# Performance work log

Hardware: AMD Instinct MI355X
Metric: run time of the kernel (lower is better)

Reference implementation:

```python
import jax, jax.numpy as jnp
import numpy as np

B, T, D_IN, D, K, H, BAND = 4, 1536, 512, 512, 2, 8, 24
DH = D // H
ALPHA, BETA, EPS = 6.0, 0.5, 1e-5


def _ln(x, g, b):
    m = x.mean(-1, keepdims=True)
    v = ((x - m) ** 2).mean(-1, keepdims=True)
    return (x - m) / jnp.sqrt(v + EPS) * g + b


def setup_inputs() -> dict:
    key = jax.random.key(0)
    ks = jax.random.split(key, 16)
    sc = 0.02
    inp = {
        "x_m": jax.random.normal(ks[0], (B, T, D_IN), jnp.float32),
        "A": jax.random.uniform(ks[1], (B, T, K), jnp.float32),
        "W_in": jax.random.normal(ks[2], (D_IN, D), jnp.float32) * sc,
        "b_in": jnp.zeros((D,), jnp.float32),
        "ln_q_g": jnp.ones((D,), jnp.float32), "ln_q_b": jnp.zeros((D,), jnp.float32),
        "ln_kv_g": jnp.ones((D,), jnp.float32), "ln_kv_b": jnp.zeros((D,), jnp.float32),
        "Wq": jax.random.normal(ks[3], (D, D), jnp.float32) * sc,
        "bq": jnp.zeros((D,), jnp.float32),
        "Wk": jax.random.normal(ks[4], (D, D), jnp.float32) * sc,
        "bk": jnp.zeros((D,), jnp.float32),
        "Wv": jax.random.normal(ks[5], (D, D), jnp.float32) * sc,
        "bv": jnp.zeros((D,), jnp.float32),
        "Wo": jax.random.normal(ks[6], (D, D), jnp.float32) * sc,
        "bo": jnp.zeros((D,), jnp.float32),
        "ln_f_g": jnp.ones((D,), jnp.float32), "ln_f_b": jnp.zeros((D,), jnp.float32),
        "W1": jax.random.normal(ks[7], (D, 4 * D), jnp.float32) * sc,
        "b1": jnp.zeros((4 * D,), jnp.float32),
        "W2": jax.random.normal(ks[8], (4 * D, D), jnp.float32) * sc,
        "b2": jnp.zeros((D,), jnp.float32),
        "ln_s_g": jnp.ones((D,), jnp.float32), "ln_s_b": jnp.zeros((D,), jnp.float32),
        "spk_tags": jax.random.normal(ks[9], (K, D), jnp.float32) / np.sqrt(D),
    }
    return inp


def reference(x_m, A, W_in, b_in, ln_q_g, ln_q_b, ln_kv_g, ln_kv_b,
              Wq, bq, Wk, bk, Wv, bv, Wo, bo,
              ln_f_g, ln_f_b, W1, b1, W2, b2, ln_s_g, ln_s_b, spk_tags):
    X = x_m @ W_in + b_in                      # [B,T,D]
    W_hat = jax.nn.sigmoid(ALPHA * (A - BETA))  # [B,T,K] sigmoid gating

    # banded additive mask (|i-j| <= BAND allowed)
    idx = jnp.arange(T)
    allowed = jnp.abs(idx[:, None] - idx[None, :]) <= BAND
    mask = jnp.where(allowed, 0.0, -jnp.inf).astype(X.dtype)  # [T,T]

    # K/V come from the (shared) mixed memory X
    KV = _ln(X, ln_kv_g, ln_kv_b)
    k_p = (KV @ Wk + bk).reshape(B, T, H, DH)
    v_p = (KV @ Wv + bv).reshape(B, T, H, DH)

    streams = []
    for kk in range(K):
        Xk = X * W_hat[..., kk:kk + 1]
        Q = _ln(Xk, ln_q_g, ln_q_b)
        q = (Q @ Wq + bq).reshape(B, T, H, DH)
        scores = jnp.einsum('bthd,bshd->bhts', q, k_p) / np.sqrt(DH) + mask
        p = jax.nn.softmax(scores, axis=-1)
        y = jnp.einsum('bhts,bshd->bthd', p, v_p).reshape(B, T, D) @ Wo + bo
        y = Xk + y                              # residual after attention
        h = _ln(y, ln_f_g, ln_f_b)
        h = jax.nn.gelu(h @ W1 + b1, approximate=False) @ W2 + b2
        out_k = y + h + spk_tags[kk]            # ffn residual + speaker tag
        out_k = _ln(out_k, ln_s_g, ln_s_b)      # per-stream LayerNorm
        streams.append(out_k)
    return jnp.concatenate(streams, axis=1)    # [B, K*T, D]
```

## Files before the change

kernel.cpp:

```cpp
#include <hip/hip_runtime.h>
#include <hip/hip_bf16.h>
#include <math.h>

#define B_    4
#define T_    1536
#define DIN_  512
#define D_    512
#define K_    2
#define H_    8
#define BAND_ 24
#define DH_   64
#define M_    (B_*T_)
#define M2_   (2*M_)
#define ALPHA_ 6.0f
#define BETA_  0.5f
#define EPS_   1e-5f

using bf8  = __attribute__((ext_vector_type(8))) short;
using f32x4 = __attribute__((ext_vector_type(4))) float;

__device__ __forceinline__ void async_copy16(const void* g, void* l) {
  __builtin_amdgcn_global_load_lds(
      (const __attribute__((address_space(1))) unsigned int*)g,
      (__attribute__((address_space(3))) unsigned int*)l, 16, 0, 0);
}

__device__ __forceinline__ short f2bf(float v) {
  __hip_bfloat16 h = (__hip_bfloat16)v;
  return *(short*)&h;
}
__device__ __forceinline__ float bf2f(short s) {
  union { unsigned u; float f; } c;
  c.u = ((unsigned)(unsigned short)s) << 16;
  return c.f;
}
__device__ __forceinline__ int swz64(int row, int col) {
  return (col & ~63) | ((((col >> 3) ^ row) & 7) << 3) | (col & 7);
}
__device__ __forceinline__ float fast_gelu(float x) {
  const float t = fmaf(0.1029504013f, x * x, 2.3021170686f);
  const float e = __builtin_amdgcn_exp2f(x * t);
  const float r = __builtin_amdgcn_rcpf(e + 1.0f);
  return fmaf(-x, r, x);
}

template<int BM, int BN, int NI, int NJ, int FLAGS>
__global__ __launch_bounds__(256) void gemm_bt_t(
    const short* __restrict__ A, const short* __restrict__ Bt,
    const float* __restrict__ bias, const void* __restrict__ res,
    const float* __restrict__ tag2,
    void* __restrict__ Cout, int M, int N, int Kd, int gx) {
  __shared__ short lA[BM * 64];
  __shared__ short lB[BN * 64];
  const int gy   = gridDim.x / gx;
  const int xcd  = blockIdx.x & 7;
  const int seq  = blockIdx.x >> 3;
  const int rpx  = gy >> 3;
  const int by   = xcd * rpx + seq / gx;
  const int bx   = seq % gx;
  const int tid  = threadIdx.x;
  const int wave = tid >> 6, lane = tid & 63;
  const int block_m = by * BM, block_n = bx * BN;
  const int wm = (wave & 1) * (BM / 2), wn = (wave >> 1) * (BN / 2);
  const int l15 = lane & 15, quad = lane >> 4, l7 = lane & 7;
  f32x4 acc[NI][NJ] = {};

  for (int k0 = 0; k0 < Kd; k0 += 64) {
    __syncthreads();
#pragma unroll
    for (int i = 0; i < BM / 32; ++i) {
      const int cb = wave * (BM * 2) + i * 64;
      const int c  = cb + lane;
      async_copy16(A + (size_t)(block_m + (c >> 3)) * Kd + k0 + (c & 7) * 8,
                   &lA[cb * 8]);
    }
#pragma unroll
    for (int i = 0; i < BN / 32; ++i) {
      const int cb = wave * (BN * 2) + i * 64;
      const int c  = cb + lane;
      async_copy16(Bt + (size_t)(block_n + (c >> 3)) * Kd + k0 + (c & 7) * 8,
                   &lB[cb * 8]);
    }
    __syncthreads();
#pragma unroll
    for (int ks = 0; ks < 2; ++ks) {
      bf8 af[NI], bfr[NJ];
#pragma unroll
      for (int i = 0; i < NI; ++i)
        af[i] = *(const bf8*)&lA[(wm + i * 16 + l15) * 64 + (((ks * 4 + quad) ^ l7) << 3)];
#pragma unroll
      for (int j = 0; j < NJ; ++j)
        bfr[j] = *(const bf8*)&lB[(wn + j * 16 + l15) * 64 + (((ks * 4 + quad) ^ l7) << 3)];
#pragma unroll
      for (int i = 0; i < NI; ++i)
#pragma unroll
        for (int j = 0; j < NJ; ++j)
          acc[i][j] = __builtin_amdgcn_mfma_f32_16x16x32_bf16(af[i], bfr[j], acc[i][j], 0, 0, 0);
    }
  }

  const int half = M >> 1;
#pragma unroll
  for (int i = 0; i < NI; ++i) {
    const int mbase = block_m + wm + i * 16 + (lane >> 4) * 4;
#pragma unroll
    for (int j = 0; j < NJ; ++j) {
      const int col = block_n + wn + j * 16 + l15;
      const float bb = bias[col];
#pragma unroll
      for (int r = 0; r < 4; ++r) {
        const int row = mbase + r;
        const size_t idx = (size_t)row * N + col;
        float v = acc[i][j][r] + bb;
        if constexpr (FLAGS & 8)  v += bf2f(((const short*)res)[idx]);
        if constexpr (FLAGS & 16) v += ((const float*)res)[idx];
        if constexpr (FLAGS & 32) v += tag2[(row >= half ? N : 0) + col];
        if constexpr (FLAGS & 1)  v = fast_gelu(v);
        if constexpr (FLAGS & 2) {
          const int oc = (FLAGS & 4) ? swz64(row, col) : col;
          ((short*)Cout)[(size_t)row * N + oc] = f2bf(v);
        } else {
          ((float*)Cout)[idx] = v;
        }
      }
    }
  }
}

__device__ __forceinline__ void tconv_tile(const float* __restrict__ W,
                                           short* __restrict__ Wt, int K, int N,
                                           int bx, int by, int tid, float (*s)[33]) {
  const int tx = tid & 31, ty = tid >> 5;
  const int k0 = by * 32, n0 = bx * 32;
#pragma unroll
  for (int r = 0; r < 4; ++r)
    s[ty * 4 + r][tx] = W[(size_t)(k0 + ty * 4 + r) * N + n0 + tx];
  __syncthreads();
#pragma unroll
  for (int r = 0; r < 4; ++r) {
    const int n = n0 + ty * 4 + r;
    Wt[(size_t)n * K + swz64(n, k0 + tx)] = f2bf(s[tx][ty * 4 + r]);
  }
}

__global__ __launch_bounds__(256) void prep_k(
    const float* __restrict__ x_m, short* __restrict__ xb,
    const float* __restrict__ W_in, short* __restrict__ WtIn,
    const float* __restrict__ Wq,  short* __restrict__ WtQ,
    const float* __restrict__ Wk,  const float* __restrict__ Wv,
    short* __restrict__ WtKV,
    const float* __restrict__ Wo,  short* __restrict__ WtO,
    const float* __restrict__ W1,  short* __restrict__ Wt1,
    const float* __restrict__ W2,  short* __restrict__ Wt2,
    const float* __restrict__ bk,  const float* __restrict__ bv,
    float* __restrict__ bkv) {
  __shared__ float s[32][33];
  const int blk = blockIdx.x, tid = threadIdx.x;
  if (blk < 3072) {
    const int e = (blk * 256 + tid) * 4;
    const int row = e >> 9, col = e & 511;
    const float4 v = *(const float4*)&x_m[e];
    short4 o;
    o.x = f2bf(v.x); o.y = f2bf(v.y); o.z = f2bf(v.z); o.w = f2bf(v.w);
    *(short4*)&xb[((size_t)row << 9) | swz64(row, col)] = o;
  } else if (blk < 3328) {
    const int t = blk - 3072; tconv_tile(W_in, WtIn, DIN_, D_, t & 15, t >> 4, tid, s);
  } else if (blk < 3584) {
    const int t = blk - 3328; tconv_tile(Wq, WtQ, D_, D_, t & 15, t >> 4, tid, s);
  } else if (blk < 3840) {
    const int t = blk - 3584; tconv_tile(Wk, WtKV, D_, D_, t & 15, t >> 4, tid, s);
  } else if (blk < 4096) {
    const int t = blk - 3840; tconv_tile(Wv, WtKV + (size_t)D_ * D_, D_, D_, t & 15, t >> 4, tid, s);
  } else if (blk < 4352) {
    const int t = blk - 4096; tconv_tile(Wo, WtO, D_, D_, t & 15, t >> 4, tid, s);
  } else if (blk < 5376) {
    const int t = blk - 4352; tconv_tile(W1, Wt1, D_, 4 * D_, t & 63, t >> 6, tid, s);
  } else if (blk < 6400) {
    const int t = blk - 5376; tconv_tile(W2, Wt2, 4 * D_, D_, t & 15, t >> 4, tid, s);
  } else {
    const int i = (blk - 6400) * 256 + tid;
    bkv[i] = (i < D_) ? bk[i] : bv[i - D_];
  }
}

__device__ __forceinline__ float block_sum(float s, float* red, int tid) {
  red[tid] = s; __syncthreads();
  for (int o = 128; o > 0; o >>= 1) {
    if (tid < o) red[tid] += red[tid + o];
    __syncthreads();
  }
  float r = red[0];
  __syncthreads();
  return r;
}

__global__ __launch_bounds__(256) void ln_bf_k(const short* __restrict__ in,
                                               const float* __restrict__ g,
                                               const float* __restrict__ b,
                                               short* __restrict__ out) {
  __shared__ float red[256];
  const int row = blockIdx.x, tid = threadIdx.x;
  const short2 xv = *(const short2*)&in[(size_t)row * D_ + 2 * tid];
  const float v0 = bf2f(xv.x), v1 = bf2f(xv.y);
  const float mean = block_sum(v0 + v1, red, tid) * (1.0f / D_);
  const float d0 = v0 - mean, d1 = v1 - mean;
  const float var = block_sum(d0 * d0 + d1 * d1, red, tid) * (1.0f / D_);
  const float inv = rsqrtf(var + EPS_);
  const float2 gg = *(const float2*)&g[2 * tid];
  const float2 bb = *(const float2*)&b[2 * tid];
  short2 o;
  o.x = f2bf(d0 * inv * gg.x + bb.x);
  o.y = f2bf(d1 * inv * gg.y + bb.y);
  *(short2*)&out[(size_t)row * D_ + swz64(row, 2 * tid)] = o;
}

__global__ __launch_bounds__(256) void scale_ln_k(
    const short* __restrict__ X, const float* __restrict__ Ain,
    const float* __restrict__ g, const float* __restrict__ b,
    short* __restrict__ Xk, short* __restrict__ out) {
  __shared__ float red[256];
  const int row = blockIdx.x, tid = threadIdx.x;
  const int kk = row / M_, rm = row % M_;
  const float a = Ain[(size_t)rm * K_ + kk];
  const float w = __builtin_amdgcn_rcpf(1.0f + __expf(-ALPHA_ * (a - BETA_)));
  const short2 xv = *(const short2*)&X[(size_t)rm * D_ + 2 * tid];
  const float v0 = bf2f(xv.x) * w, v1 = bf2f(xv.y) * w;
  short2 xo; xo.x = f2bf(v0); xo.y = f2bf(v1);
  *(short2*)&Xk[(size_t)row * D_ + 2 * tid] = xo;
  const float mean = block_sum(v0 + v1, red, tid) * (1.0f / D_);
  const float d0 = v0 - mean, d1 = v1 - mean;
  const float var = block_sum(d0 * d0 + d1 * d1, red, tid) * (1.0f / D_);
  const float inv = rsqrtf(var + EPS_);
  const float2 gg = *(const float2*)&g[2 * tid];
  const float2 bb = *(const float2*)&b[2 * tid];
  short2 o;
  o.x = f2bf(d0 * inv * gg.x + bb.x);
  o.y = f2bf(d1 * inv * gg.y + bb.y);
  *(short2*)&out[(size_t)row * D_ + swz64(row, 2 * tid)] = o;
}

__global__ __launch_bounds__(256) void final_ln_k(
    const short* __restrict__ t2, const float* __restrict__ g,
    const float* __restrict__ b, float* __restrict__ out) {
  __shared__ float red[256];
  const int row = blockIdx.x, tid = threadIdx.x;
  const int kk = row / M_, rm = row % M_;
  const int bb_ = rm / T_, t = rm % T_;
  const size_t orow = (size_t)bb_ * (K_ * T_) + (size_t)kk * T_ + t;
  const short2 xv = *(const short2*)&t2[(size_t)row * D_ + 2 * tid];
  const float v0 = bf2f(xv.x), v1 = bf2f(xv.y);
  const float mean = block_sum(v0 + v1, red, tid) * (1.0f / D_);
  const float d0 = v0 - mean, d1 = v1 - mean;
  const float var = block_sum(d0 * d0 + d1 * d1, red, tid) * (1.0f / D_);
  const float inv = rsqrtf(var + EPS_);
  const float2 gg = *(const float2*)&g[2 * tid];
  const float2 bb = *(const float2*)&b[2 * tid];
  float2 o;
  o.x = d0 * inv * gg.x + bb.x;
  o.y = d1 * inv * gg.y + bb.y;
  *(float2*)&out[orow * D_ + 2 * tid] = o;
}

#define QT_  64
#define KT_  (QT_ + 2 * BAND_)
#define SKQ_ 72
#define STV_ 136
__global__ __launch_bounds__(256) void attn_mfma_k(
    const short* __restrict__ q, const short* __restrict__ KVp,
    short* __restrict__ out) {
  __shared__ short sK[KT_ * SKQ_];
  __shared__ short sQ[QT_ * SKQ_];
  __shared__ short sVt[DH_ * STV_];
  __shared__ short sP[4][16 * SKQ_];
  const int t0 = blockIdx.x * QT_;
  const int h  = blockIdx.y;
  const int z  = blockIdx.z;
  const int b  = z % B_;
  const int tid = threadIdx.x;
  const int wave = tid >> 6, lane = tid & 63;
  const int rr = tid >> 5, c2 = tid & 31;

  for (int r0 = 0; r0 < KT_; r0 += 8) {
    const int r = r0 + rr;
    const int s = t0 - BAND_ + r;
    short2 kv = {0, 0}, vv = {0, 0};
    if (s >= 0 && s < T_) {
      const size_t g = (size_t)(b * T_ + s) * (2 * D_) + h * DH_ + c2 * 2;
      kv = *(const short2*)&KVp[g];
      vv = *(const short2*)&KVp[g + D_];
    }
    *(short2*)&sK[r * SKQ_ + c2 * 2] = kv;
    sVt[(c2 * 2)     * STV_ + r] = vv.x;
    sVt[(c2 * 2 + 1) * STV_ + r] = vv.y;
  }
  for (int r0 = 0; r0 < QT_; r0 += 8) {
    const int r = r0 + rr;
    const size_t g = (size_t)(z * T_ + t0 + r) * D_ + h * DH_ + c2 * 2;
    *(short2*)&sQ[r * SKQ_ + c2 * 2] = *(const short2*)&q[g];
  }
  __syncthreads();

  const int qg  = wave * 16;
  const int l15 = lane & 15, quad = lane >> 4;

  bf8 qa0 = *(const bf8*)&sQ[(qg + l15) * SKQ_ + quad * 8];
  bf8 qa1 = *(const bf8*)&sQ[(qg + l15) * SKQ_ + 32 + quad * 8];
  f32x4 acc[4];
#pragma unroll
  for (int j = 0; j < 4; ++j) {
    const bf8 kb0 = *(const bf8*)&sK[(qg + j * 16 + l15) * SKQ_ + quad * 8];
    const bf8 kb1 = *(const bf8*)&sK[(qg + j * 16 + l15) * SKQ_ + 32 + quad * 8];
    f32x4 z4 = {0.f, 0.f, 0.f, 0.f};
    acc[j] = __builtin_amdgcn_mfma_f32_16x16x32_bf16(qa0, kb0, z4, 0, 0, 0);
    acc[j] = __builtin_amdgcn_mfma_f32_16x16x32_bf16(qa1, kb1, acc[j], 0, 0, 0);
  }

#pragma unroll
  for (int reg = 0; reg < 4; ++reg) {
    const int i = quad * 4 + reg;
    float sc[4];
    float mx = -1e30f;
#pragma unroll
    for (int j = 0; j < 4; ++j) {
      const int c = j * 16 + l15;
      const int s = t0 + qg - BAND_ + c;
      const int rel = c - i;
      const bool valid = (rel >= 0) && (rel <= 2 * BAND_) && (s >= 0) && (s < T_);
      sc[j] = valid ? acc[j][reg] * 0.125f : -1e30f;
      mx = fmaxf(mx, sc[j]);
    }
    for (int o = 1; o < 16; o <<= 1) mx = fmaxf(mx, __shfl_xor(mx, o));
    float p[4], se = 0.0f;
#pragma unroll
    for (int j = 0; j < 4; ++j) {
      p[j] = (sc[j] > -1e29f) ? __expf(sc[j] - mx) : 0.0f;
      se += p[j];
    }
    for (int o = 1; o < 16; o <<= 1) se += __shfl_xor(se, o);
    const float inv = __builtin_amdgcn_rcpf(se);
#pragma unroll
    for (int j = 0; j < 4; ++j)
      sP[wave][i * SKQ_ + j * 16 + l15] = f2bf(p[j] * inv);
  }

  const bf8 pa0 = *(const bf8*)&sP[wave][l15 * SKQ_ + quad * 8];
  const bf8 pa1 = *(const bf8*)&sP[wave][l15 * SKQ_ + 32 + quad * 8];
  f32x4 oacc[4] = {};
#pragma unroll
  for (int dt = 0; dt < 4; ++dt) {
    const bf8 vb0 = *(const bf8*)&sVt[(dt * 16 + l15) * STV_ + qg + quad * 8];
    const bf8 vb1 = *(const bf8*)&sVt[(dt * 16 + l15) * STV_ + qg + 32 + quad * 8];
    oacc[dt] = __builtin_amdgcn_mfma_f32_16x16x32_bf16(pa0, vb0, oacc[dt], 0, 0, 0);
    oacc[dt] = __builtin_amdgcn_mfma_f32_16x16x32_bf16(pa1, vb1, oacc[dt], 0, 0, 0);
  }
#pragma unroll
  for (int dt = 0; dt < 4; ++dt)
#pragma unroll
    for (int reg = 0; reg < 4; ++reg) {
      const int i = quad * 4 + reg;
      const int row = t0 + qg + i;
      const int col = h * DH_ + dt * 16 + l15;
      out[(size_t)(z * T_ + row) * D_ + swz64(row, col)] = f2bf(oacc[dt][reg]);
    }
}

extern "C" void kernel_launch(void* const* d_in, const int* in_sizes, int n_in,
                              void* d_out, int out_size, void* d_ws, size_t ws_size,
                              hipStream_t stream) {
  const float* x_m    = (const float*)d_in[0];
  const float* A      = (const float*)d_in[1];
  const float* W_in   = (const float*)d_in[2];
  const float* b_in   = (const float*)d_in[3];
  const float* ln_q_g = (const float*)d_in[4];
  const float* ln_q_b = (const float*)d_in[5];
  const float* ln_kv_g= (const float*)d_in[6];
  const float* ln_kv_b= (const float*)d_in[7];
  const float* Wq     = (const float*)d_in[8];
  const float* bq     = (const float*)d_in[9];
  const float* Wk     = (const float*)d_in[10];
  const float* bk     = (const float*)d_in[11];
  const float* Wv     = (const float*)d_in[12];
  const float* bv     = (const float*)d_in[13];
  const float* Wo     = (const float*)d_in[14];
  const float* bo     = (const float*)d_in[15];
  const float* ln_f_g = (const float*)d_in[16];
  const float* ln_f_b = (const float*)d_in[17];
  const float* W1     = (const float*)d_in[18];
  const float* b1     = (const float*)d_in[19];
  const float* W2     = (const float*)d_in[20];
  const float* b2     = (const float*)d_in[21];
  const float* ln_s_g = (const float*)d_in[22];
  const float* ln_s_b = (const float*)d_in[23];
  const float* tags   = (const float*)d_in[24];
  float* out = (float*)d_out;

  const size_t MD = (size_t)M_ * D_;
  float* bkv = (float*)d_ws;
  short* X    = (short*)(bkv + 1024);
  short* Xk2  = X    + MD;
  short* LNb2 = Xk2  + 2 * MD;
  short* qb2  = LNb2 + 2 * MD;
  short* KVpb = qb2  + 2 * MD;
  short* T2b  = KVpb + 2 * MD;
  short* H1b  = T2b  + 2 * MD;
  short* WtIn = H1b + (size_t)M2_ * 4 * D_;
  short* WtQ  = WtIn + (size_t)D_ * DIN_;
  short* WtKV = WtQ  + (size_t)D_ * D_;
  short* WtO  = WtKV + (size_t)2 * D_ * D_;
  short* Wt1  = WtO  + (size_t)D_ * D_;
  short* Wt2  = Wt1  + (size_t)4 * D_ * D_;
  short* xb   = qb2;
  short* KVb  = LNb2;

  prep_k<<<6404, 256, 0, stream>>>(x_m, xb, W_in, WtIn, Wq, WtQ, Wk, Wv, WtKV,
                                   Wo, WtO, W1, Wt1, W2, Wt2, bk, bv, bkv);

  gemm_bt_t<128,64,4,2, 2><<<(D_/64) * (M_/128), 256, 0, stream>>>(
      xb, WtIn, b_in, nullptr, nullptr, X, M_, D_, DIN_, D_/64);
  ln_bf_k<<<M_, 256, 0, stream>>>(X, ln_kv_g, ln_kv_b, KVb);
  gemm_bt_t<128,128,4,4, 2><<<((2*D_)/128) * (M_/128), 256, 0, stream>>>(
      KVb, WtKV, bkv, nullptr, nullptr, KVpb, M_, 2*D_, D_, (2*D_)/128);

  scale_ln_k<<<M2_, 256, 0, stream>>>(X, A, ln_q_g, ln_q_b, Xk2, LNb2);
  gemm_bt_t<128,128,4,4, 2><<<(D_/128) * (M2_/128), 256, 0, stream>>>(
      LNb2, WtQ, bq, nullptr, nullptr, qb2, M2_, D_, D_, D_/128);
  attn_mfma_k<<<dim3(T_/QT_, H_, B_*K_), 256, 0, stream>>>(qb2, KVpb, LNb2);
  gemm_bt_t<128,128,4,4, 2|8><<<(D_/128) * (M2_/128), 256, 0, stream>>>(
      LNb2, WtO, bo, Xk2, nullptr, Xk2, M2_, D_, D_, D_/128);
  ln_bf_k<<<M2_, 256, 0, stream>>>(Xk2, ln_f_g, ln_f_b, LNb2);
  gemm_bt_t<128,64,4,2, 1|2|4><<<((4*D_)/64) * (M2_/128), 256, 0, stream>>>(
      LNb2, Wt1, b1, nullptr, nullptr, H1b, M2_, 4*D_, D_, (4*D_)/64);
  gemm_bt_t<128,64,4,2, 2|8|32><<<(D_/64) * (M2_/128), 256, 0, stream>>>(
      H1b, Wt2, b2, Xk2, tags, T2b, M2_, D_, 4*D_, D_/64);
  final_ln_k<<<M2_, 256, 0, stream>>>(T2b, ln_s_g, ln_s_b, out);
}
```

Measured before the change: 319.0 us.

## Add 256x256-tile 8-wave GEMM with ping-pong pipelining for FFN up-projection

```diff
diff --git a/kernel.cpp b/kernel.cpp
--- a/kernel.cpp
+++ b/kernel.cpp
@@ -125,6 +125,159 @@
       }
     }
   }
+}
+
+template<int FLAGS>
+__global__ __launch_bounds__(512, 2) void gemm8_t(
+    const short* __restrict__ A, const short* __restrict__ Bt,
+    const float* __restrict__ bias, const void* __restrict__ res,
+    const float* __restrict__ tag2,
+    void* __restrict__ Cout, int M, int N, int Kd, int gx) {
+  __shared__ short lA[2][256 * 64];
+  __shared__ short lB[2][256 * 64];
+  const int gy   = gridDim.x / gx;
+  const int xcd  = blockIdx.x & 7;
+  const int seq  = blockIdx.x >> 3;
+  const int rpx  = gy >> 3;
+  const int by   = xcd * rpx + seq / gx;
+  const int bx   = seq % gx;
+  const int tid  = threadIdx.x;
+  const int wave = tid >> 6, lane = tid & 63;
+  const int block_m = by * 256, block_n = bx * 256;
+  const int wm2 = (wave & 1) * 64;
+  const int wn2 = (wave >> 1) * 32;
+  const int l15 = lane & 15, quad = lane >> 4, l7 = lane & 7;
+  const int kq0 = ((quad ^ l7) << 3), kq1 = (((4 + quad) ^ l7) << 3);
+
+  const int ca  = wave * 128 + lane;
+  const int ra0 = ca >> 3, ka0 = (ca & 7) * 8;
+  const int cb2 = ca + 64;
+  const int ra1 = cb2 >> 3, ka1 = (cb2 & 7) * 8;
+
+  f32x4 acc[8][4] = {};
+  bf8 aF[4][2], bF[4][2];
+
+#define STG8(LDSP, GBASE, ROWB, K0)                                           \
+  { async_copy16((GBASE) + (size_t)((ROWB) + ra0) * Kd + (K0) + ka0,          \
+                 (LDSP) + ca * 8);                                            \
+    async_copy16((GBASE) + (size_t)((ROWB) + ra1) * Kd + (K0) + ka1,          \
+                 (LDSP) + cb2 * 8); }
+
+#define RDA8(BUF, IH)                                                         \
+  { const short* p_ = (BUF) + (IH) * 8192;                                    \
+    _Pragma("unroll")                                                         \
+    for (int i = 0; i < 4; ++i) {                                             \
+      const int rw_ = (wm2 + i * 16 + l15) * 64;                              \
+      aF[i][0] = *(const bf8*)&p_[rw_ + kq0];                                 \
+      aF[i][1] = *(const bf8*)&p_[rw_ + kq1];                                 \
+    } }
+
+#define RDB8(BUF, JH)                                                         \
+  { const short* p_ = (BUF) + (JH) * 8192;                                    \
+    _Pragma("unroll")                                                         \
+    for (int j = 0; j < 2; ++j) {                                             \
+      const int rw_ = (wn2 + j * 16 + l15) * 64;                              \
+      bF[(JH) * 2 + j][0] = *(const bf8*)&p_[rw_ + kq0];                      \
+      bF[(JH) * 2 + j][1] = *(const bf8*)&p_[rw_ + kq1];                      \
+    } }
+
+#define MM8(IH, JH)                                                           \
+  _Pragma("unroll")                                                           \
+  for (int i = 0; i < 4; ++i)                                                 \
+  _Pragma("unroll")                                                           \
+  for (int j = 0; j < 2; ++j) {                                               \
+    acc[(IH)*4+i][(JH)*2+j] = __builtin_amdgcn_mfma_f32_16x16x32_bf16(        \
+        aF[i][0], bF[(JH)*2+j][0], acc[(IH)*4+i][(JH)*2+j], 0, 0, 0);         \
+    acc[(IH)*4+i][(JH)*2+j] = __builtin_amdgcn_mfma_f32_16x16x32_bf16(        \
+        aF[i][1], bF[(JH)*2+j][1], acc[(IH)*4+i][(JH)*2+j], 0, 0, 0);         \
+  }
+
+#define WAITV8 asm volatile("s_waitcnt vmcnt(4)" ::: "memory")
+#define WAITL8 do { asm volatile("s_waitcnt lgkmcnt(0)" ::: "memory");        \
+                    __builtin_amdgcn_sched_barrier(0); } while (0)
+
+  const int NT = Kd >> 6;
+  STG8(&lA[0][0],    A,  block_m,       0);
+  STG8(&lB[0][0],    Bt, block_n,       0);
+  STG8(&lB[0][8192], Bt, block_n + 128, 0);
+  STG8(&lA[0][8192], A,  block_m + 128, 0);
+  if (NT > 1) STG8(&lA[1][0], A, block_m, 64);
+  WAITV8;
+  __builtin_amdgcn_s_barrier();
+
+  int cur = 0;
+  for (int t = 0; t < NT; ++t) {
+    const int nb = cur ^ 1;
+    const int k1 = (t + 1) << 6, k2 = (t + 2) << 6;
+    const short* cA = lA[cur];
+    const short* cB = lB[cur];
+    const bool m1 = (t + 1 < NT), m2 = (t + 2 < NT);
+    WAITV8;
+    RDA8(cA, 0); RDB8(cB, 0);
+    if (m1) STG8(&lB[nb][0], Bt, block_n, k1);
+    __builtin_amdgcn_s_barrier();
+    WAITL8;
+    __builtin_amdgcn_s_setprio(1); MM8(0, 0); __builtin_amdgcn_s_setprio(0);
+    __builtin_amdgcn_s_barrier();
+    WAITV8;
+    RDB8(cB, 1);
+    if (m1) STG8(&lB[nb][8192], Bt, block_n + 128, k1);
+    __builtin_amdgcn_s_barrier();
+    WAITL8;
+    __builtin_amdgcn_s_setprio(1); MM8(0, 1); __builtin_amdgcn_s_setprio(0);
+    __builtin_amdgcn_s_barrier();
+    WAITV8;
+    RDA8(cA, 1);
+    if (m1) STG8(&lA[nb][8192], A, block_m + 128, k1);
+    __builtin_amdgcn_s_barrier();
+    WAITL8;
+    __builtin_amdgcn_s_setprio(1); MM8(1, 1); __builtin_amdgcn_s_setprio(0);
+    __builtin_amdgcn_s_barrier();
+    WAITV8;
+    if (m2) STG8(&lA[cur][0], A, block_m, k2);
+    __builtin_amdgcn_s_barrier();
+    WAITL8;
+    __builtin_amdgcn_s_setprio(1); MM8(1, 0); __builtin_amdgcn_s_setprio(0);
+    __builtin_amdgcn_s_barrier();
+    cur = nb;
+  }
+
+  const int half = M >> 1;
+#pragma unroll
+  for (int ih = 0; ih < 2; ++ih)
+#pragma unroll
+  for (int i = 0; i < 4; ++i) {
+    const int mbase = block_m + wm2 + ih * 128 + i * 16 + quad * 4;
+#pragma unroll
+    for (int jh = 0; jh < 2; ++jh)
+#pragma unroll
+    for (int j = 0; j < 2; ++j) {
+      const int col = block_n + wn2 + jh * 128 + j * 16 + l15;
+      const float bb = bias[col];
+#pragma unroll
+      for (int r = 0; r < 4; ++r) {
+        const int row = mbase + r;
+        const size_t idx = (size_t)row * N + col;
+        float v = acc[ih * 4 + i][jh * 2 + j][r] + bb;
+        if constexpr (FLAGS & 8)  v += bf2f(((const short*)res)[idx]);
+        if constexpr (FLAGS & 16) v += ((const float*)res)[idx];
+        if constexpr (FLAGS & 32) v += tag2[(row >= half ? N : 0) + col];
+        if constexpr (FLAGS & 1)  v = fast_gelu(v);
+        if constexpr (FLAGS & 2) {
+          const int oc = (FLAGS & 4) ? swz64(row, col) : col;
+          ((short*)Cout)[(size_t)row * N + oc] = f2bf(v);
+        } else {
+          ((float*)Cout)[idx] = v;
+        }
+      }
+    }
+  }
+#undef STG8
+#undef RDA8
+#undef RDB8
+#undef MM8
+#undef WAITV8
+#undef WAITL8
 }
 
 __device__ __forceinline__ void tconv_tile(const float* __restrict__ W,
@@ -428,8 +581,8 @@
   gemm_bt_t<128,128,4,4, 2|8><<<(D_/128) * (M2_/128), 256, 0, stream>>>(
       LNb2, WtO, bo, Xk2, nullptr, Xk2, M2_, D_, D_, D_/128);
   ln_bf_k<<<M2_, 256, 0, stream>>>(Xk2, ln_f_g, ln_f_b, LNb2);
-  gemm_bt_t<128,64,4,2, 1|2|4><<<((4*D_)/64) * (M2_/128), 256, 0, stream>>>(
-      LNb2, Wt1, b1, nullptr, nullptr, H1b, M2_, 4*D_, D_, (4*D_)/64);
+  gemm8_t<1|2|4><<<((4*D_)/256) * (M2_/256), 512, 0, stream>>>(
+      LNb2, Wt1, b1, nullptr, nullptr, H1b, M2_, 4*D_, D_, (4*D_)/256);
   gemm_bt_t<128,64,4,2, 2|8|32><<<(D_/64) * (M2_/128), 256, 0, stream>>>(
       H1b, Wt2, b2, Xk2, tags, T2b, M2_, D_, 4*D_, D_/64);
   final_ln_k<<<M2_, 256, 0, stream>>>(T2b, ln_s_g, ln_s_b, out);
```

Result: slower. 328.1 us (+2.9%).
